# Kernel optimization log

Hardware: AMD Instinct MI355X
Metric: run time of the kernel (lower is better)

The kernel has to match this reference:

```python
import math
import jax, jax.numpy as jnp
import numpy as np

V, S, D, H, HID, L, B = 32000, 1024, 768, 12, 3072, 4, 2
HD = D // H
EPS = 1e-5
CLAMP = 1e9


def setup_inputs() -> dict:
    key = jax.random.key(0)
    ks = jax.random.split(key, 10)
    std = 0.02
    return {
        "W_emb": jax.random.normal(ks[0], (V, D), jnp.float32) * std,      # tied with lm_head
        "pos_emb": jax.random.normal(ks[1], (S, D), jnp.float32) * std,
        "norm1_g": jnp.ones((L, D), jnp.float32),
        "norm1_b": jnp.zeros((L, D), jnp.float32),
        "qkv_w": jax.random.normal(ks[2], (L, 3 * D, D), jnp.float32) * std,
        "qkv_b": jnp.zeros((L, 3 * D), jnp.float32),
        "proj_w": jax.random.normal(ks[3], (L, D, D), jnp.float32) * std,
        "proj_b": jnp.zeros((L, D), jnp.float32),
        "norm2_g": jnp.ones((L, D), jnp.float32),
        "norm2_b": jnp.zeros((L, D), jnp.float32),
        "ffn_w1": jax.random.normal(ks[4], (L, HID, D), jnp.float32) * std,
        "ffn_b1": jnp.zeros((L, HID), jnp.float32),
        "ffn_w2": jax.random.normal(ks[5], (L, D, HID), jnp.float32) * std,
        "ffn_b2": jnp.zeros((L, D), jnp.float32),
        "fin_g": jnp.ones((D,), jnp.float32),
        "fin_b": jnp.zeros((D,), jnp.float32),
        "input_ids": jax.random.randint(ks[6], (B, S), 0, V, jnp.int64),
    }


def layer_norm(x, g, b):
    mean = jnp.mean(x, axis=-1, keepdims=True)
    var = jnp.mean((x - mean) ** 2, axis=-1, keepdims=True)
    return g * ((x - mean) / jnp.sqrt(var + EPS)) + b


def attention(x, qkv_w, qkv_b, proj_w, proj_b):
    b, s, _ = x.shape
    qkv = x @ qkv_w.T + qkv_b                                  # [B,S,3D]
    qkv = qkv.reshape(b, s, H, 3 * HD).transpose(0, 2, 1, 3)   # [B,H,S,3*HD]
    q, k, v = qkv[..., :HD], qkv[..., HD:2 * HD], qkv[..., 2 * HD:]
    scaled = jnp.einsum("bhqd,bhkd->bhqk", q, k) / math.sqrt(HD)
    mask = jnp.tril(jnp.ones((s, s), bool))
    scaled = jnp.clip(jnp.where(mask, scaled, -jnp.inf), -CLAMP, CLAMP)
    attn = jax.nn.softmax(scaled, axis=-1)
    vals = jnp.einsum("bhqk,bhkd->bhqd", attn, v)
    vals = vals.transpose(0, 2, 1, 3).reshape(b, s, D)
    return vals @ proj_w.T + proj_b


def reference(W_emb, pos_emb, norm1_g, norm1_b, qkv_w, qkv_b, proj_w, proj_b,
              norm2_g, norm2_b, ffn_w1, ffn_b1, ffn_w2, ffn_b2, fin_g, fin_b,
              input_ids):
    x = W_emb[input_ids] * math.sqrt(D)          # [B,S,D]
    x = x + pos_emb[None, :x.shape[1], :]
    for i in range(L):
        h = layer_norm(x, norm1_g[i], norm1_b[i])
        x = x + attention(h, qkv_w[i], qkv_b[i], proj_w[i], proj_b[i])
        h = layer_norm(x, norm2_g[i], norm2_b[i])
        h = jax.nn.gelu(h @ ffn_w1[i].T + ffn_b1[i], approximate=False)
        x = x + h @ ffn_w2[i].T + ffn_b2[i]
    x = layer_norm(x, fin_g, fin_b)
    logits = x @ W_emb.T                         # tied lm_head, no bias
    return logits
```

## Files before the change

### kernel.cpp

```cpp
#include <hip/hip_runtime.h>
#include <hip/hip_bf16.h>
#include <math.h>

typedef __bf16 bf16_t;
typedef __bf16 bf16x8 __attribute__((ext_vector_type(8)));
typedef float f32x4 __attribute__((ext_vector_type(4)));

__device__ __forceinline__ void gload16(const bf16_t* g, bf16_t* l) {
  __builtin_amdgcn_global_load_lds(
      (const __attribute__((address_space(1))) unsigned int*)g,
      (__attribute__((address_space(3))) unsigned int*)l, 16, 0, 0);
}


template<int EPI>
__global__ __launch_bounds__(128, 3) void gemm_bt(
    const bf16_t* __restrict__ A, const bf16_t* __restrict__ W,
    const float* __restrict__ bias,
    bf16_t* __restrict__ obf, float* __restrict__ of32,
    int M, int N, int K, int kLen)
{
  __shared__ bf16_t As[128 * 64];
  __shared__ bf16_t Bs[64 * 64];
  const int tid  = threadIdx.x;
  const int lane = tid & 63;
  const int w    = tid >> 6;
  const long m0 = (long)blockIdx.y * 128;
  const long n0 = (long)blockIdx.x * 64;
  const int k0 = blockIdx.z * kLen;
  const int k1 = k0 + kLen;

  f32x4 acc[4][4] = {};

  const int l7  = lane & 7;
  const int l15 = lane & 15;
  const int hi  = lane >> 4;
  const int rA  = w * 64 + l15;

  for (int kt = k0; kt < k1; kt += 64) {
#pragma unroll
    for (int i = 0; i < 8; ++i) {
      const int cl  = tid + i * 128;
      const int row = cl >> 3;
      const int j   = (cl & 7) ^ (row & 7);
      gload16(A + (m0 + row) * K + kt + (j << 3), As + cl * 8);
    }
#pragma unroll
    for (int i = 0; i < 4; ++i) {
      const int cl  = tid + i * 128;
      const int row = cl >> 3;
      const int j   = (cl & 7) ^ (row & 7);
      gload16(W + (n0 + row) * K + kt + (j << 3), Bs + cl * 8);
    }
    __syncthreads();
#pragma unroll
    for (int kk = 0; kk < 64; kk += 32) {
      const int ck = ((((kk >> 3) + hi) ^ l7) << 3);
      bf16x8 af[4], bfr[4];
#pragma unroll
      for (int m = 0; m < 4; ++m) af[m]  = *(const bf16x8*)(As + (rA + m * 16) * 64 + ck);
#pragma unroll
      for (int n = 0; n < 4; ++n) bfr[n] = *(const bf16x8*)(Bs + (l15 + n * 16) * 64 + ck);
#pragma unroll
      for (int m = 0; m < 4; ++m)
#pragma unroll
        for (int n = 0; n < 4; ++n)
          acc[m][n] = __builtin_amdgcn_mfma_f32_16x16x32_bf16(af[m], bfr[n], acc[m][n], 0, 0, 0);
    }
    __syncthreads();
  }

  const int lr = hi << 2;
#pragma unroll
  for (int n = 0; n < 4; ++n) {
    const long gcol = n0 + n * 16 + l15;
    float bv = 0.f;
    if (EPI == 0 || EPI == 1) bv = bias[gcol];
    if (EPI == 4 && k0 == 0)  bv = bias[gcol];
#pragma unroll
    for (int m = 0; m < 4; ++m) {
      const long grow0 = m0 + w * 64 + m * 16 + lr;
#pragma unroll
      for (int r = 0; r < 4; ++r) {
        float v = acc[m][n][r] + bv;
        const long idx = (grow0 + r) * N + gcol;
        if (EPI == 0) {
          obf[idx] = (bf16_t)v;
        } else if (EPI == 1) {
          v = 0.5f * v * (1.0f + erff(v * 0.70710678118654752f));
          obf[idx] = (bf16_t)v;
        } else {
          atomicAdd(&of32[idx], v);
        }
      }
    }
  }
}

__global__ __launch_bounds__(256, 2) void gemm_logits(
    const bf16_t* __restrict__ A, const bf16_t* __restrict__ W,
    float* __restrict__ out)
{
  __shared__ bf16_t As[128 * 64];
  __shared__ bf16_t Bs[128 * 64];
  const int tid  = threadIdx.x;
  const int lane = tid & 63;
  const int w    = tid >> 6;
  const int wr   = w >> 1;
  const int wc   = w & 1;
  const int d    = blockIdx.x;
  const int wk   = (d & 7) * 500 + (d >> 3);
  const long m0  = (long)(wk & 15) * 128;
  const long n0  = (long)(wk >> 4) * 128;
  const int K = 768, N = 32000;

  f32x4 acc[4][4] = {};
  const int l7  = lane & 7;
  const int l15 = lane & 15;
  const int hi  = lane >> 4;
  const int rA  = wr * 64 + l15;
  const int rB  = wc * 64 + l15;

  for (int kt = 0; kt < K; kt += 64) {
#pragma unroll
    for (int i = 0; i < 4; ++i) {
      const int cl  = tid + i * 256;
      const int row = cl >> 3;
      const int j   = (cl & 7) ^ (row & 7);
      gload16(A + (m0 + row) * K + kt + (j << 3), As + cl * 8);
    }
#pragma unroll
    for (int i = 0; i < 4; ++i) {
      const int cl  = tid + i * 256;
      const int row = cl >> 3;
      const int j   = (cl & 7) ^ (row & 7);
      gload16(W + (n0 + row) * K + kt + (j << 3), Bs + cl * 8);
    }
    __syncthreads();
#pragma unroll
    for (int kk = 0; kk < 64; kk += 32) {
      const int ck = ((((kk >> 3) + hi) ^ l7) << 3);
      bf16x8 af[4], bfr[4];
#pragma unroll
      for (int m = 0; m < 4; ++m) af[m]  = *(const bf16x8*)(As + (rA + m * 16) * 64 + ck);
#pragma unroll
      for (int n = 0; n < 4; ++n) bfr[n] = *(const bf16x8*)(Bs + (rB + n * 16) * 64 + ck);
#pragma unroll
      for (int m = 0; m < 4; ++m)
#pragma unroll
        for (int n = 0; n < 4; ++n)
          acc[m][n] = __builtin_amdgcn_mfma_f32_16x16x32_bf16(af[m], bfr[n], acc[m][n], 0, 0, 0);
    }
    __syncthreads();
  }

  const int lr = hi << 2;
#pragma unroll
  for (int n = 0; n < 4; ++n) {
    const long gcol = n0 + wc * 64 + n * 16 + l15;
#pragma unroll
    for (int m = 0; m < 4; ++m) {
      const long grow0 = m0 + wr * 64 + m * 16 + lr;
#pragma unroll
      for (int r = 0; r < 4; ++r)
        out[(grow0 + r) * N + gcol] = acc[m][n][r];
    }
  }
}

__global__ __launch_bounds__(256) void vtrans_kernel(
    const bf16_t* __restrict__ qkv, bf16_t* __restrict__ vT)
{
  __shared__ bf16_t T[128][72];
  const int bh = blockIdx.x;
  const int b = bh / 12, h = bh % 12;
  const int s0 = blockIdx.y * 128;
  const int tid = threadIdx.x;
  const bf16_t* src = qkv + (long)(b * 1024 + s0) * 2304 + h * 192 + 128;
#pragma unroll
  for (int i = 0; i < 4; ++i) {
    const int row = i * 32 + (tid >> 3);
    const int c = (tid & 7) * 8;
    *(bf16x8*)&T[row][c] = *(const bf16x8*)(src + (long)row * 2304 + c);
  }
  __syncthreads();
  const int dd = tid >> 2;
  const int sq = (tid & 3) * 32;
  bf16_t* dst = vT + ((long)bh * 64 + dd) * 1024 + s0 + sq;
#pragma unroll
  for (int j2 = 0; j2 < 4; ++j2) {
    bf16x8 o;
#pragma unroll
    for (int j = 0; j < 8; ++j) o[j] = T[sq + j2 * 8 + j][dd];
    *(bf16x8*)(dst + j2 * 8) = o;
  }
}

__global__ __launch_bounds__(256) void attn_kernel(
    const bf16_t* __restrict__ qkv, const bf16_t* __restrict__ vT,
    bf16_t* __restrict__ aout)
{
  __shared__ bf16_t Plds[4][16 * 64];
  const int tid  = threadIdx.x;
  const int lane = tid & 63;
  const int w    = tid >> 6;
  const int wid  = blockIdx.x * 4 + w;
  const int qt   = wid & 63;
  const int bh   = wid >> 6;
  const int b    = bh / 12;
  const int h    = bh % 12;
  const int q0   = qt << 4;

  const bf16_t* base = qkv + (long)b * 1024 * 2304 + h * 192;
  const bf16_t* vtb  = vT + (long)bh * 64 * 1024;
  const int koff  = (lane >> 4) << 3;
  const int l15   = lane & 15;
  const int rbase = (lane >> 4) << 2;

  const bf16x8 qf0 = *(const bf16x8*)(base + (long)(q0 + l15) * 2304 + koff);
  const bf16x8 qf1 = *(const bf16x8*)(base + (long)(q0 + l15) * 2304 + 32 + koff);

  f32x4 acc[4] = {};
  float mrun[4], lrun[4];
#pragma unroll
  for (int r = 0; r < 4; ++r) { mrun[r] = -1e30f; lrun[r] = 0.f; }

  bf16_t* pl = &Plds[w][0];
  const int kbmax = (q0 + 15) >> 6;
  for (int kb = 0; kb <= kbmax; ++kb) {
    const int kv0 = kb << 6;
    const f32x4 z = {0.f, 0.f, 0.f, 0.f};
    f32x4 s[4];
    __builtin_amdgcn_s_setprio(1);
#pragma unroll
    for (int g = 0; g < 4; ++g) {
      const bf16_t* kr = base + 64 + (long)(kv0 + g * 16 + l15) * 2304;
      const bf16x8 ka = *(const bf16x8*)(kr + koff);
      const bf16x8 kb2 = *(const bf16x8*)(kr + 32 + koff);
      s[g] = __builtin_amdgcn_mfma_f32_16x16x32_bf16(qf0, ka, z, 0, 0, 0);
      s[g] = __builtin_amdgcn_mfma_f32_16x16x32_bf16(qf1, kb2, s[g], 0, 0, 0);
    }
    __builtin_amdgcn_s_setprio(0);

#pragma unroll
    for (int r = 0; r < 4; ++r) {
      const int qi = q0 + rbase + r;
      float v[4];
#pragma unroll
      for (int g = 0; g < 4; ++g)
        v[g] = (kv0 + g * 16 + l15 <= qi) ? s[g][r] * 0.125f : -1e9f;
      float mx = fmaxf(fmaxf(v[0], v[1]), fmaxf(v[2], v[3]));
#pragma unroll
      for (int dd = 1; dd < 16; dd <<= 1) mx = fmaxf(mx, __shfl_xor(mx, dd));
      const float mnew = fmaxf(mrun[r], mx);
      const float sc = __expf(mrun[r] - mnew);
      float p[4], sm = 0.f;
#pragma unroll
      for (int g = 0; g < 4; ++g) { p[g] = __expf(v[g] - mnew); sm += p[g]; }
#pragma unroll
      for (int dd = 1; dd < 16; dd <<= 1) sm += __shfl_xor(sm, dd);
      lrun[r] = lrun[r] * sc + sm;
      mrun[r] = mnew;
      acc[0][r] *= sc; acc[1][r] *= sc; acc[2][r] *= sc; acc[3][r] *= sc;
#pragma unroll
      for (int g = 0; g < 4; ++g)
        pl[(rbase + r) * 64 + g * 16 + l15] = (bf16_t)p[g];
    }
    asm volatile("s_waitcnt lgkmcnt(0)" ::: "memory");
    const bf16x8 pf0 = *(const bf16x8*)(pl + l15 * 64 + koff);
    const bf16x8 pf1 = *(const bf16x8*)(pl + l15 * 64 + 32 + koff);
    __builtin_amdgcn_s_setprio(1);
#pragma unroll
    for (int hh = 0; hh < 2; ++hh) {
      const bf16x8 pf = hh ? pf1 : pf0;
      const int sbase = kv0 + hh * 32 + koff;
#pragma unroll
      for (int cb = 0; cb < 4; ++cb) {
        const bf16x8 vf = *(const bf16x8*)(vtb + (long)(cb * 16 + l15) * 1024 + sbase);
        acc[cb] = __builtin_amdgcn_mfma_f32_16x16x32_bf16(pf, vf, acc[cb], 0, 0, 0);
      }
    }
    __builtin_amdgcn_s_setprio(0);
  }

#pragma unroll
  for (int cb = 0; cb < 4; ++cb)
#pragma unroll
    for (int r = 0; r < 4; ++r) {
      const float o = acc[cb][r] / lrun[r];
      aout[(long)(b * 1024 + q0 + rbase + r) * 768 + h * 64 + cb * 16 + l15] = (bf16_t)o;
    }
}

__global__ __launch_bounds__(256) void ln_kernel(
    const float* __restrict__ x, const float* __restrict__ g,
    const float* __restrict__ bta, bf16_t* __restrict__ out)
{
  const int row = blockIdx.x;
  const int tid = threadIdx.x;
  const float* xr = x + (long)row * 768;
  const float v0 = xr[tid], v1 = xr[tid + 256], v2 = xr[tid + 512];
  float s  = v0 + v1 + v2;
  float ss = v0 * v0 + v1 * v1 + v2 * v2;
#pragma unroll
  for (int d = 1; d < 64; d <<= 1) { s += __shfl_xor(s, d); ss += __shfl_xor(ss, d); }
  __shared__ float sh[8];
  const int lane = tid & 63, wv = tid >> 6;
  if (lane == 0) { sh[wv] = s; sh[4 + wv] = ss; }
  __syncthreads();
  s  = sh[0] + sh[1] + sh[2] + sh[3];
  ss = sh[4] + sh[5] + sh[6] + sh[7];
  const float mean = s * (1.0f / 768.0f);
  const float var  = ss * (1.0f / 768.0f) - mean * mean;
  const float inv  = rsqrtf(var + 1e-5f);
  bf16_t* orow = out + (long)row * 768;
  orow[tid]       = (bf16_t)(g[tid]       * ((v0 - mean) * inv) + bta[tid]);
  orow[tid + 256] = (bf16_t)(g[tid + 256] * ((v1 - mean) * inv) + bta[tid + 256]);
  orow[tid + 512] = (bf16_t)(g[tid + 512] * ((v2 - mean) * inv) + bta[tid + 512]);
}

__global__ __launch_bounds__(256) void embed_kernel(
    const int* __restrict__ ids, const float* __restrict__ We,
    const float* __restrict__ pos, float* __restrict__ x)
{
  const int row = blockIdx.x;
  const int tid = threadIdx.x;
  const int s = row & 1023;
  const long id = ids[row];
  const float* wr = We + id * 768;
  const float* pr = pos + (long)s * 768;
  float* xr = x + (long)row * 768;
#pragma unroll
  for (int k = 0; k < 3; ++k) {
    const int c = tid + k * 256;
    xr[c] = wr[c] * 27.712812921102035f + pr[c];
  }
}

__global__ __launch_bounds__(256) void cvt_kernel(
    const float* __restrict__ in, bf16_t* __restrict__ out, long n)
{
  const long i = ((long)blockIdx.x * 256 + threadIdx.x) * 8;
  if (i >= n) return;
  bf16x8 o;
#pragma unroll
  for (int j = 0; j < 8; ++j) o[j] = (bf16_t)in[i + j];
  *(bf16x8*)(out + i) = o;
}

extern "C" void kernel_launch(void* const* d_in, const int* in_sizes, int n_in,
                              void* d_out, int out_size, void* d_ws, size_t ws_size,
                              hipStream_t stream)
{
  const float* W_emb = (const float*)d_in[0];
  const float* pos   = (const float*)d_in[1];
  const float* n1g   = (const float*)d_in[2];
  const float* n1b   = (const float*)d_in[3];
  const float* qkvw  = (const float*)d_in[4];
  const float* qkvb  = (const float*)d_in[5];
  const float* projw = (const float*)d_in[6];
  const float* projb = (const float*)d_in[7];
  const float* n2g   = (const float*)d_in[8];
  const float* n2b   = (const float*)d_in[9];
  const float* f1w   = (const float*)d_in[10];
  const float* f1b   = (const float*)d_in[11];
  const float* f2w   = (const float*)d_in[12];
  const float* f2b   = (const float*)d_in[13];
  const float* fing  = (const float*)d_in[14];
  const float* finb  = (const float*)d_in[15];
  const int*   ids   = (const int*)d_in[16];
  float* out = (float*)d_out;

  char* ws = (char*)d_ws;
  float*  x     = (float*)(ws);
  bf16_t* h     = (bf16_t*)(ws + 6291456);
  bf16_t* qkv   = (bf16_t*)(ws + 9437184);
  bf16_t* attn  = (bf16_t*)(ws + 18874368);
  bf16_t* ffn1o = (bf16_t*)(ws + 22020096);
  bf16_t* Wq    = (bf16_t*)(ws + 34603008);
  bf16_t* Wp    = (bf16_t*)(ws + 48758784);
  bf16_t* W1    = (bf16_t*)(ws + 53477376);
  bf16_t* W2    = (bf16_t*)(ws + 72351744);
  bf16_t* We    = (bf16_t*)(ws + 91226112);
  bf16_t* vT    = (bf16_t*)(ws + 140378112);

  cvt_kernel<<<dim3(3456),  256, 0, stream>>>(qkvw,  Wq, 4L * 2304 * 768);
  cvt_kernel<<<dim3(1152),  256, 0, stream>>>(projw, Wp, 4L * 768 * 768);
  cvt_kernel<<<dim3(4608),  256, 0, stream>>>(f1w,   W1, 4L * 3072 * 768);
  cvt_kernel<<<dim3(4608),  256, 0, stream>>>(f2w,   W2, 4L * 768 * 3072);
  cvt_kernel<<<dim3(12000), 256, 0, stream>>>(W_emb, We, 32000L * 768);

  embed_kernel<<<2048, 256, 0, stream>>>(ids, W_emb, pos, x);

  for (int i = 0; i < 4; ++i) {
    ln_kernel<<<2048, 256, 0, stream>>>(x, n1g + i * 768, n1b + i * 768, h);
    gemm_bt<0><<<dim3(36, 16), 128, 0, stream>>>(
        h, Wq + (long)i * 2304 * 768, qkvb + i * 2304, qkv, nullptr, 2048, 2304, 768, 768);
    vtrans_kernel<<<dim3(24, 8), 256, 0, stream>>>(qkv, vT);
    attn_kernel<<<384, 256, 0, stream>>>(qkv, vT, attn);
    gemm_bt<4><<<dim3(12, 16, 2), 128, 0, stream>>>(
        attn, Wp + (long)i * 768 * 768, projb + i * 768, nullptr, x, 2048, 768, 768, 384);
    ln_kernel<<<2048, 256, 0, stream>>>(x, n2g + i * 768, n2b + i * 768, h);
    gemm_bt<1><<<dim3(48, 16), 128, 0, stream>>>(
        h, W1 + (long)i * 3072 * 768, f1b + i * 3072, ffn1o, nullptr, 2048, 3072, 768, 768);
    gemm_bt<4><<<dim3(12, 16, 4), 128, 0, stream>>>(
        ffn1o, W2 + (long)i * 768 * 3072, f2b + i * 768, nullptr, x, 2048, 768, 3072, 768);
  }
  ln_kernel<<<2048, 256, 0, stream>>>(x, fing, finb, h);
  gemm_logits<<<dim3(4000), 256, 0, stream>>>(h, We, out);
}
```

Before: 887.5 us.

## Rewrite logits GEMM as 256x256 tile, 8-wave, double-buffered pipelined kernel

Replaces the 128x128 four-wave logits GEMM with a 256x256-tile, eight-wave kernel. It double-buffers the A and B tiles in LDS, preloading two k-steps ahead and waiting with explicit vmcnt counts. Each wave computes its 128x64 output in four quadrant phases with barriers, setprio and sched_barrier so that LDS reads and global prefetches overlap the MFMA work. The larger tile raises operand reuse and cuts global traffic, but LDS use grows to 128KB per block, which limits occupancy, and the hand-tuned waitcnt and barrier schedule could be fragile.

Measured after the change: 906.5 us. +2.1%, slower.

```diff
diff --git a/kernel.cpp b/kernel.cpp
--- a/kernel.cpp
+++ b/kernel.cpp
@@ -97,73 +97,156 @@
   }
 }
 
-__global__ __launch_bounds__(256, 2) void gemm_logits(
+__global__ __launch_bounds__(512, 2) void gemm_logits8(
     const bf16_t* __restrict__ A, const bf16_t* __restrict__ W,
     float* __restrict__ out)
 {
-  __shared__ bf16_t As[128 * 64];
-  __shared__ bf16_t Bs[128 * 64];
+  __shared__ bf16_t Abuf[2][2][128 * 64];
+  __shared__ bf16_t Bbuf[2][2][128 * 64];
   const int tid  = threadIdx.x;
   const int lane = tid & 63;
   const int w    = tid >> 6;
-  const int wr   = w >> 1;
-  const int wc   = w & 1;
+  const int wm   = w >> 2;
+  const int wn   = w & 3;
   const int d    = blockIdx.x;
-  const int wk   = (d & 7) * 500 + (d >> 3);
-  const long m0  = (long)(wk & 15) * 128;
-  const long n0  = (long)(wk >> 4) * 128;
+  const int wk   = (d & 7) * 125 + (d >> 3);
+  const long m0  = (long)(wk & 7) * 256;
+  const long n0  = (long)(wk >> 3) * 256;
   const int K = 768, N = 32000;
 
-  f32x4 acc[4][4] = {};
-  const int l7  = lane & 7;
-  const int l15 = lane & 15;
-  const int hi  = lane >> 4;
-  const int rA  = wr * 64 + l15;
-  const int rB  = wc * 64 + l15;
-
-  for (int kt = 0; kt < K; kt += 64) {
-#pragma unroll
-    for (int i = 0; i < 4; ++i) {
-      const int cl  = tid + i * 256;
+  const int l7 = lane & 7, l15 = lane & 15, hi = lane >> 4;
+
+  auto stageA = [&](int t, int h) {
+#pragma unroll
+    for (int i = 0; i < 2; ++i) {
+      const int cl  = tid + i * 512;
       const int row = cl >> 3;
       const int j   = (cl & 7) ^ (row & 7);
-      gload16(A + (m0 + row) * K + kt + (j << 3), As + cl * 8);
-    }
-#pragma unroll
-    for (int i = 0; i < 4; ++i) {
-      const int cl  = tid + i * 256;
+      gload16(A + (m0 + h * 128 + row) * K + t * 64 + (j << 3),
+              &Abuf[t & 1][h][cl * 8]);
+    }
+  };
+  auto stageB = [&](int t, int h) {
+#pragma unroll
+    for (int i = 0; i < 2; ++i) {
+      const int cl  = tid + i * 512;
       const int row = cl >> 3;
       const int j   = (cl & 7) ^ (row & 7);
-      gload16(W + (n0 + row) * K + kt + (j << 3), Bs + cl * 8);
-    }
-    __syncthreads();
-#pragma unroll
-    for (int kk = 0; kk < 64; kk += 32) {
-      const int ck = ((((kk >> 3) + hi) ^ l7) << 3);
-      bf16x8 af[4], bfr[4];
-#pragma unroll
-      for (int m = 0; m < 4; ++m) af[m]  = *(const bf16x8*)(As + (rA + m * 16) * 64 + ck);
-#pragma unroll
-      for (int n = 0; n < 4; ++n) bfr[n] = *(const bf16x8*)(Bs + (rB + n * 16) * 64 + ck);
-#pragma unroll
-      for (int m = 0; m < 4; ++m)
-#pragma unroll
-        for (int n = 0; n < 4; ++n)
-          acc[m][n] = __builtin_amdgcn_mfma_f32_16x16x32_bf16(af[m], bfr[n], acc[m][n], 0, 0, 0);
-    }
-    __syncthreads();
-  }
-
-  const int lr = hi << 2;
-#pragma unroll
-  for (int n = 0; n < 4; ++n) {
-    const long gcol = n0 + wc * 64 + n * 16 + l15;
-#pragma unroll
-    for (int m = 0; m < 4; ++m) {
-      const long grow0 = m0 + wr * 64 + m * 16 + lr;
+      gload16(W + (n0 + h * 128 + row) * K + t * 64 + (j << 3),
+              &Bbuf[t & 1][h][cl * 8]);
+    }
+  };
+
+  f32x4 acc[8][4] = {};
+  bf16x8 areg[4][2], breg[4][2];
+
+  stageA(0, 0); stageA(0, 1); stageB(0, 0); stageB(0, 1);
+  stageA(1, 0); stageA(1, 1); stageB(1, 0); stageB(1, 1);
+
+  const int rbB = (wn & 1) * 64;
+
+  for (int t = 0; t < 12; ++t) {
+    const int buf = t & 1;
+    if (t < 11) asm volatile("s_waitcnt vmcnt(8)" ::: "memory");
+    else        asm volatile("s_waitcnt vmcnt(0)" ::: "memory");
+    __builtin_amdgcn_s_barrier();
+    const bf16_t* Ab = &Abuf[buf][wm][0];
+    const bf16_t* Bb = &Bbuf[buf][wn >> 1][0];
+
+#pragma unroll
+    for (int kkI = 0; kkI < 2; ++kkI) {
+      const int ck = ((((kkI << 2) + hi) ^ l7) << 3);
+#pragma unroll
+      for (int mq = 0; mq < 4; ++mq)
+        areg[mq][kkI] = *(const bf16x8*)(Ab + (mq * 16 + l15) * 64 + ck);
+#pragma unroll
+      for (int nq = 0; nq < 2; ++nq)
+        breg[nq][kkI] = *(const bf16x8*)(Bb + (rbB + nq * 16 + l15) * 64 + ck);
+    }
+    __builtin_amdgcn_s_barrier();
+    __builtin_amdgcn_s_setprio(1);
+#pragma unroll
+    for (int mq = 0; mq < 4; ++mq)
+#pragma unroll
+      for (int nq = 0; nq < 2; ++nq)
+#pragma unroll
+        for (int kkI = 0; kkI < 2; ++kkI)
+          acc[mq][nq] = __builtin_amdgcn_mfma_f32_16x16x32_bf16(
+              areg[mq][kkI], breg[nq][kkI], acc[mq][nq], 0, 0, 0);
+    __builtin_amdgcn_s_setprio(0);
+    asm volatile("s_waitcnt lgkmcnt(0)" ::: "memory");
+    __builtin_amdgcn_sched_barrier(0);
+    __builtin_amdgcn_s_barrier();
+
+#pragma unroll
+    for (int kkI = 0; kkI < 2; ++kkI) {
+      const int ck = ((((kkI << 2) + hi) ^ l7) << 3);
+#pragma unroll
+      for (int nq = 0; nq < 2; ++nq)
+        breg[2 + nq][kkI] = *(const bf16x8*)(Bb + (rbB + 32 + nq * 16 + l15) * 64 + ck);
+    }
+    __builtin_amdgcn_s_barrier();
+    __builtin_amdgcn_s_setprio(1);
+#pragma unroll
+    for (int mq = 0; mq < 4; ++mq)
+#pragma unroll
+      for (int nq = 0; nq < 2; ++nq)
+#pragma unroll
+        for (int kkI = 0; kkI < 2; ++kkI)
+          acc[mq][2 + nq] = __builtin_amdgcn_mfma_f32_16x16x32_bf16(
+              areg[mq][kkI], breg[2 + nq][kkI], acc[mq][2 + nq], 0, 0, 0);
+    __builtin_amdgcn_s_setprio(0);
+    asm volatile("s_waitcnt lgkmcnt(0)" ::: "memory");
+    __builtin_amdgcn_sched_barrier(0);
+    __builtin_amdgcn_s_barrier();
+
+#pragma unroll
+    for (int kkI = 0; kkI < 2; ++kkI) {
+      const int ck = ((((kkI << 2) + hi) ^ l7) << 3);
+#pragma unroll
+      for (int mq = 0; mq < 4; ++mq)
+        areg[mq][kkI] = *(const bf16x8*)(Ab + (64 + mq * 16 + l15) * 64 + ck);
+    }
+    if (t + 2 < 12) { stageB(t + 2, 0); stageB(t + 2, 1); }
+    __builtin_amdgcn_s_barrier();
+    __builtin_amdgcn_s_setprio(1);
+#pragma unroll
+    for (int mq = 0; mq < 4; ++mq)
+#pragma unroll
+      for (int nq = 0; nq < 2; ++nq)
+#pragma unroll
+        for (int kkI = 0; kkI < 2; ++kkI)
+          acc[4 + mq][2 + nq] = __builtin_amdgcn_mfma_f32_16x16x32_bf16(
+              areg[mq][kkI], breg[2 + nq][kkI], acc[4 + mq][2 + nq], 0, 0, 0);
+    __builtin_amdgcn_s_setprio(0);
+    asm volatile("s_waitcnt lgkmcnt(0)" ::: "memory");
+    __builtin_amdgcn_sched_barrier(0);
+    __builtin_amdgcn_s_barrier();
+
+    if (t + 2 < 12) { stageA(t + 2, 0); stageA(t + 2, 1); }
+    __builtin_amdgcn_s_barrier();
+    __builtin_amdgcn_s_setprio(1);
+#pragma unroll
+    for (int mq = 0; mq < 4; ++mq)
+#pragma unroll
+      for (int nq = 0; nq < 2; ++nq)
+#pragma unroll
+        for (int kkI = 0; kkI < 2; ++kkI)
+          acc[4 + mq][nq] = __builtin_amdgcn_mfma_f32_16x16x32_bf16(
+              areg[mq][kkI], breg[nq][kkI], acc[4 + mq][nq], 0, 0, 0);
+    __builtin_amdgcn_s_setprio(0);
+    __builtin_amdgcn_sched_barrier(0);
+  }
+
+#pragma unroll
+  for (int mi = 0; mi < 8; ++mi) {
+    const long grow0 = m0 + wm * 128 + mi * 16 + hi * 4;
+#pragma unroll
+    for (int ni = 0; ni < 4; ++ni) {
+      const long gcol = n0 + wn * 64 + ni * 16 + l15;
 #pragma unroll
       for (int r = 0; r < 4; ++r)
-        out[(grow0 + r) * N + gcol] = acc[m][n][r];
+        out[(grow0 + r) * N + gcol] = acc[mi][ni][r];
     }
   }
 }
@@ -407,5 +490,5 @@
         ffn1o, W2 + (long)i * 768 * 3072, f2b + i * 768, nullptr, x, 2048, 768, 3072, 768);
   }
   ln_kernel<<<2048, 256, 0, stream>>>(x, fing, finb, h);
-  gemm_logits<<<dim3(4000), 256, 0, stream>>>(h, We, out);
-}
+  gemm_logits8<<<dim3(1000), 512, 0, stream>>>(h, We, out);
+}
```
